# Kernel tuning notes

Measured on AMD Instinct MI355X. Metric: run time of the kernel, lower is better.

The kernel has to match this reference:

```python
import jax, jax.numpy as jnp
import numpy as np

B, S, D, H = 8, 1024, 1024, 16
HD = D // H  # head dim 64

def setup_inputs() -> dict:
    key = jax.random.key(0)
    ks = jax.random.split(key, 7)
    def w(k):
        return jax.random.normal(k, (D, D), dtype=jnp.float32) * (1.0 / np.sqrt(D))
    return {
        'q': jax.random.normal(ks[0], (B, S, D), dtype=jnp.float32),
        'k': jax.random.normal(ks[1], (B, S, D), dtype=jnp.float32),
        'v': jax.random.normal(ks[2], (B, S, D), dtype=jnp.float32),
        'Wq': w(ks[3]), 'Wk': w(ks[4]), 'Wv': w(ks[5]), 'Wo': w(ks[6]),
    }

def reference(q, k, v, Wq, Wk, Wv, Wo):
    # projections (nn.Linear, no bias): y = x @ W.T
    def heads(x, W):
        return (x @ W.T).reshape(B, S, H, HD)
    qh, kh, vh = heads(q, Wq), heads(k, Wk), heads(v, Wv)
    scale = 1.0 / np.sqrt(HD).astype(np.float32)
    scores = jnp.einsum('bqhd,bkhd->bhqk', qh, kh) * scale  # [B,H,S,S]
    # masked=True -> causal mask
    causal = jnp.tril(jnp.ones((S, S), dtype=bool))
    scores = jnp.where(causal[None, None], scores, jnp.float32(-1e9))
    attn = jax.nn.softmax(scores, axis=-1)
    out = jnp.einsum('bhqk,bkhd->bqhd', attn, vh).reshape(B, S, D)
    return out @ Wo.T
```

## Files before the change

kernel.cpp:

```cpp
#include <hip/hip_runtime.h>
#include <hip/hip_bf16.h>

#define B_ 8
#define S_ 1024
#define D_ 1024
#define H_ 16
#define HD_ 64
#define M_ (B_*S_)
#define NQB (S_/128)

typedef __attribute__((ext_vector_type(8))) short short8;
typedef __attribute__((ext_vector_type(4))) short short4v;
typedef __attribute__((ext_vector_type(4))) float f32x4;
typedef __attribute__((ext_vector_type(16))) float f32x16;
typedef __attribute__((ext_vector_type(4))) int int4v;
typedef __attribute__((ext_vector_type(2))) int int2v;

#define CSC 0.18033688f

__device__ __forceinline__ unsigned short f2bf(float f) {
    unsigned int u = __float_as_uint(f);
    u += 0x7FFF + ((u >> 16) & 1);
    return (unsigned short)(u >> 16);
}

__device__ __forceinline__ void gload16(const void* g, void* l) {
    __builtin_amdgcn_global_load_lds(
        (const __attribute__((address_space(1))) void*)g,
        (__attribute__((address_space(3))) void*)l, 16, 0, 0);
}

__device__ __forceinline__ int2v plswap(int a, int b) {
    return __builtin_amdgcn_permlane32_swap(a, b, false, false);
}

__device__ __forceinline__ float max3f(float a, float b, float c) {
    return fmaxf(fmaxf(a, b), c);
}

struct CvtArgs { const float* src[28]; unsigned short* dst[28]; };

__global__ __launch_bounds__(256)
void cvt_w(CvtArgs a)
{
    const int y = blockIdx.y;
    const float* __restrict__ src = a.src[y];
    unsigned short* __restrict__ dst = a.dst[y];
    int i = blockIdx.x * 256 + threadIdx.x;
    float4 x = reinterpret_cast<const float4*>(src)[i*2];
    float4 z = reinterpret_cast<const float4*>(src)[i*2+1];
    short8 v = short8{(short)f2bf(x.x),(short)f2bf(x.y),(short)f2bf(x.z),(short)f2bf(x.w),
                      (short)f2bf(z.x),(short)f2bf(z.y),(short)f2bf(z.z),(short)f2bf(z.w)};
    reinterpret_cast<short8*>(dst)[i] = v;
}

__device__ __forceinline__ void gemm_core_bf16A(
    const unsigned short* __restrict__ A, const unsigned short* __restrict__ Wb,
    short* lds, int m0, int n0, int tid, f32x4 (&acc)[4][4])
{
    const int K = D_;
    const int lane = tid & 63, wave = tid >> 6;
    const int wr = wave >> 1, wc = wave & 1;
    const int r16 = lane & 15, g4 = lane >> 4;
    const int srow = lane >> 3;
    const int scol = ((lane ^ srow) & 7) * 8;

    #define STAGE(t, bi)                                                      \
        { _Pragma("unroll")                                                   \
          for (int c = 0; c < 4; ++c) {                                       \
              int chunk = wave*4 + c;                                         \
              gload16(Wb + (size_t)(n0 + chunk*8 + srow) * K + (t)*64 + scol, \
                      lds + (bi)*16384 + 8192 + chunk*512);                   \
              gload16(A + (size_t)(m0 + chunk*8 + srow) * K + (t)*64 + scol,  \
                      lds + (bi)*16384 + chunk*512);                          \
          } }

    STAGE(0, 0);

    const int NT = K / 64;
    for (int t = 0; t < NT; ++t) {
        const int cur = t & 1;
        if (t + 1 < NT) {
            STAGE(t+1, cur^1);
            asm volatile("s_waitcnt vmcnt(8)" ::: "memory");
        } else {
            asm volatile("s_waitcnt vmcnt(0)" ::: "memory");
        }
        __builtin_amdgcn_s_barrier();

        const short* Ab = lds + cur*16384;
        const short* Bb = Ab + 8192;
        #pragma unroll
        for (int ks = 0; ks < 2; ++ks) {
            short8 af[4], bf[4];
            #pragma unroll
            for (int m = 0; m < 4; ++m) {
                int r = wr*64 + m*16 + r16;
                af[m] = *reinterpret_cast<const short8*>(
                    &Ab[r*64 + (((ks*4 + g4) ^ (r16 & 7)) << 3)]);
            }
            #pragma unroll
            for (int n = 0; n < 4; ++n) {
                int r = wc*64 + n*16 + r16;
                bf[n] = *reinterpret_cast<const short8*>(
                    &Bb[r*64 + (((ks*4 + g4) ^ (r16 & 7)) << 3)]);
            }
            __builtin_amdgcn_s_setprio(1);
            #pragma unroll
            for (int m = 0; m < 4; ++m)
                #pragma unroll
                for (int n = 0; n < 4; ++n)
                    acc[m][n] = __builtin_amdgcn_mfma_f32_16x16x32_bf16(af[m], bf[n], acc[m][n], 0, 0, 0);
            __builtin_amdgcn_s_setprio(0);
        }
        __builtin_amdgcn_s_barrier();
    }
    #undef STAGE
}

template<int MODE>
__device__ __forceinline__ void epilogue_vec(
    float* Cl, void* __restrict__ Ov, int m0, int n0, int tid, f32x4 (&acc)[4][4])
{
    const int N = D_;
    const int lane = tid & 63, wave = tid >> 6;
    const int wr = wave >> 1, wc = wave & 1;
    const int r16 = lane & 15, g4 = lane >> 4;

    #pragma unroll
    for (int p = 0; p < 2; ++p) {
        if (p) __syncthreads();
        if (wr == p) {
            #pragma unroll
            for (int m = 0; m < 4; ++m)
                #pragma unroll
                for (int n = 0; n < 4; ++n)
                    #pragma unroll
                    for (int i = 0; i < 4; ++i)
                        Cl[(m*16 + g4*4 + i)*132 + wc*64 + n*16 + r16] = acc[m][n][i];
        }
        __syncthreads();
        if (MODE == 1) {
            #pragma unroll
            for (int j = 0; j < 8; ++j) {
                int c = j*256 + tid;
                int row = c >> 5, cg = c & 31;
                float4 val = *reinterpret_cast<const float4*>(&Cl[row*132 + cg*4]);
                *reinterpret_cast<float4*>(
                    &((float*)Ov)[(size_t)(m0 + p*64 + row)*N + n0 + cg*4]) = val;
            }
        } else {
            #pragma unroll
            for (int j = 0; j < 4; ++j) {
                int c2 = j*256 + tid;
                int row = c2 >> 4, col = (c2 & 15)*8;
                float4 a = *reinterpret_cast<const float4*>(&Cl[row*132 + col]);
                float4 bq = *reinterpret_cast<const float4*>(&Cl[row*132 + col + 4]);
                if (MODE == 3) {
                    a.x *= CSC; a.y *= CSC; a.z *= CSC; a.w *= CSC;
                    bq.x *= CSC; bq.y *= CSC; bq.z *= CSC; bq.w *= CSC;
                }
                short8 v = short8{(short)f2bf(a.x),(short)f2bf(a.y),(short)f2bf(a.z),(short)f2bf(a.w),
                                  (short)f2bf(bq.x),(short)f2bf(bq.y),(short)f2bf(bq.z),(short)f2bf(bq.w)};
                *reinterpret_cast<short8*>(
                    &((unsigned short*)Ov)[(size_t)(m0 + p*64 + row)*N + n0 + col]) = v;
            }
        }
    }
}

struct ProjArgs {
    const unsigned short* A[3];
    const unsigned short* W[3];
    void* O[3];
};

__global__ __launch_bounds__(256)
void gemm_proj(ProjArgs pa)
{
    __shared__ __align__(16) short lds[32768];

    const int L = blockIdx.x;
    const int which = L >> 9;
    const int inner = L & 511;
    const int xcd = inner & 7, jj = inner >> 3;
    const int m0 = ((xcd << 3) | (jj & 7)) * 128;
    const int n0 = (jj >> 3) * 128;
    const int tid = threadIdx.x;

    f32x4 acc[4][4] = {};
    gemm_core_bf16A(pa.A[which], pa.W[which], lds, m0, n0, tid, acc);

    if (which == 2) {
        const int lane = tid & 63, wave = tid >> 6;
        const int wr = wave >> 1, wc = wave & 1;
        const int r16 = lane & 15, g4 = lane >> 4;
        #pragma unroll
        for (int m = 0; m < 4; ++m) {
            int row0 = m0 + wr*64 + m*16 + g4*4;
            #pragma unroll
            for (int n = 0; n < 4; ++n) {
                int col = n0 + wc*64 + n*16 + r16;
                size_t vrow = (size_t)((row0 >> 10)*16 + (col >> 6))*64 + (col & 63);
                short4v pk = short4v{(short)f2bf(acc[m][n][0]), (short)f2bf(acc[m][n][1]),
                                     (short)f2bf(acc[m][n][2]), (short)f2bf(acc[m][n][3])};
                *reinterpret_cast<short4v*>((unsigned short*)pa.O[2] + vrow*S_ + (row0 & 1023)) = pk;
            }
        }
    } else if (which == 0) {
        epilogue_vec<3>((float*)lds, pa.O[0], m0, n0, tid, acc);
    } else {
        epilogue_vec<0>((float*)lds, pa.O[1], m0, n0, tid, acc);
    }
}

__global__ __launch_bounds__(256)
void gemm_final(const unsigned short* __restrict__ A, const unsigned short* __restrict__ Wb,
                float* __restrict__ Ov)
{
    __shared__ __align__(16) short lds[32768];

    const int L = blockIdx.x;
    const int xcd = L & 7, jj = L >> 3;
    const int m0 = ((xcd << 3) | (jj & 7)) * 128;
    const int n0 = (jj >> 3) * 128;
    const int tid = threadIdx.x;

    f32x4 acc[4][4] = {};
    gemm_core_bf16A(A, Wb, lds, m0, n0, tid, acc);
    epilogue_vec<1>((float*)lds, Ov, m0, n0, tid, acc);
}

__global__ __launch_bounds__(256)
void attn_fwd(const unsigned short* __restrict__ Qh,
              const unsigned short* __restrict__ Kh,
              const unsigned short* __restrict__ VtG,
              unsigned short* __restrict__ AO)
{
    __shared__ __align__(16) short Kl[2][64*64];
    __shared__ __align__(16) short Vl[2][64*64];

    const int tid  = threadIdx.x;
    const int lane = tid & 63, wave = tid >> 6;
    const int l31 = lane & 31, h32 = lane >> 5;
    const int L = blockIdx.x;
    const int xcd = L & 7, jj = L >> 3;
    const int pr = jj & 3;
    const int hb = xcd*16 + (jj >> 2);
    const int h = hb & 15, b = hb >> 4;

    const int slot = tid & 7;
    const int r0 = tid >> 3, r1 = r0 + 32;
    const int koff0 = r0*64 + ((slot ^ (r0 & 7)) << 3);
    const int koff1 = r1*64 + ((slot ^ (r1 & 7)) << 3);

    const unsigned short* Kg0 = Kh + ((size_t)b*S_)*D_ + h*HD_;
    const unsigned short* Vg0 = VtG + ((size_t)(b*H_ + h)*HD_)*S_;

    for (int t = 0; t < 2; ++t) {
        const int qb = t ? pr : (NQB - 1 - pr);
        const int q0w = qb*128 + wave*32;
        const int qi  = q0w + l31;

        short8 qf[4];
        #pragma unroll
        for (int m = 0; m < 4; ++m)
            qf[m] = *reinterpret_cast<const short8*>(
                Qh + ((size_t)b*S_ + qi)*D_ + h*HD_ + m*16 + h32*8);

        f32x16 o0 = {}, o1 = {};
        float mrow = -1e30f, lsum = 0.f;
        const int nkb = 2*qb + 2;

        short8 ka, kc, va, vc;
        ka = *reinterpret_cast<const short8*>(Kg0 + (size_t)r0*D_ + slot*8);
        kc = *reinterpret_cast<const short8*>(Kg0 + (size_t)r1*D_ + slot*8);
        va = *reinterpret_cast<const short8*>(Vg0 + (size_t)r0*S_ + slot*8);
        vc = *reinterpret_cast<const short8*>(Vg0 + (size_t)r1*S_ + slot*8);
        *reinterpret_cast<short8*>(&Kl[0][koff0]) = ka;
        *reinterpret_cast<short8*>(&Kl[0][koff1]) = kc;
        *reinterpret_cast<short8*>(&Vl[0][koff0]) = va;
        *reinterpret_cast<short8*>(&Vl[0][koff1]) = vc;
        __syncthreads();

        for (int kb = 0; kb < nkb; ++kb) {
            const int cur = kb & 1;
            const bool havenext = (kb + 1 < nkb);
            if (havenext) {
                const unsigned short* Kg = Kg0 + (size_t)(kb+1)*64*D_;
                const unsigned short* Vg = Vg0 + (kb+1)*64;
                ka = *reinterpret_cast<const short8*>(Kg + (size_t)r0*D_ + slot*8);
                kc = *reinterpret_cast<const short8*>(Kg + (size_t)r1*D_ + slot*8);
                va = *reinterpret_cast<const short8*>(Vg + (size_t)r0*S_ + slot*8);
                vc = *reinterpret_cast<const short8*>(Vg + (size_t)r1*S_ + slot*8);
            }

            if (kb*64 <= q0w + 31) {
                f32x16 p0 = {}, p1 = {};
                __builtin_amdgcn_s_setprio(1);
                #pragma unroll
                for (int m = 0; m < 4; ++m) {
                    short8 kf0 = *reinterpret_cast<const short8*>(
                        &Kl[cur][l31*64 + ((((m<<1)|h32) ^ (l31 & 7)) << 3)]);
                    short8 kf1 = *reinterpret_cast<const short8*>(
                        &Kl[cur][(32 + l31)*64 + ((((m<<1)|h32) ^ (l31 & 7)) << 3)]);
                    p0 = __builtin_amdgcn_mfma_f32_32x32x16_bf16(kf0, qf[m], p0, 0, 0, 0);
                    p1 = __builtin_amdgcn_mfma_f32_32x32x16_bf16(kf1, qf[m], p1, 0, 0, 0);
                }
                __builtin_amdgcn_s_setprio(0);

                if (kb*64 + 63 > q0w) {
                    #pragma unroll
                    for (int r = 0; r < 16; ++r) {
                        int kk = (r & 3) + ((r >> 2) << 3) + (h32 << 2);
                        if (kb*64      + kk > qi) p0[r] = -1e30f;
                        if (kb*64 + 32 + kk > qi) p1[r] = -1e30f;
                    }
                }

                float t0 = max3f(p0[0],  p0[1],  p0[2]);
                float t1 = max3f(p0[3],  p0[4],  p0[5]);
                float t2 = max3f(p0[6],  p0[7],  p0[8]);
                float t3 = max3f(p0[9],  p0[10], p0[11]);
                float t4 = max3f(p0[12], p0[13], p0[14]);
                float t5 = max3f(p0[15], p1[0],  p1[1]);
                float t6 = max3f(p1[2],  p1[3],  p1[4]);
                float t7 = max3f(p1[5],  p1[6],  p1[7]);
                float t8 = max3f(p1[8],  p1[9],  p1[10]);
                float t9 = max3f(p1[11], p1[12], p1[13]);
                float ta = fmaxf(p1[14], p1[15]);
                float mloc = fmaxf(max3f(max3f(t0,t1,t2), max3f(t3,t4,t5), max3f(t6,t7,t8)),
                                   fmaxf(t9, ta));
                int2v mm = plswap(__float_as_int(mloc), __float_as_int(mloc));
                float pm = fmaxf(__int_as_float(mm.x), __int_as_float(mm.y));

                if (__any(pm > mrow + 11.5416f)) {
                    float mn = fmaxf(mrow, pm);
                    float so = exp2f(mrow - mn);
                    #pragma unroll
                    for (int r = 0; r < 16; ++r) { o0[r] *= so; o1[r] *= so; }
                    lsum *= so;
                    mrow = mn;
                }

                #pragma unroll
                for (int r = 0; r < 16; ++r) p0[r] = exp2f(p0[r] - mrow);
                #pragma unroll
                for (int r = 0; r < 16; ++r) p1[r] = exp2f(p1[r] - mrow);
                float sq[8];
                #pragma unroll
                for (int r = 0; r < 8; ++r)
                    sq[r] = (p0[2*r] + p0[2*r+1]) + (p1[2*r] + p1[2*r+1]);
                float rs = ((sq[0]+sq[1]) + (sq[2]+sq[3])) + ((sq[4]+sq[5]) + (sq[6]+sq[7]));
                int2v ss = plswap(__float_as_int(rs), __float_as_int(rs));
                lsum += __int_as_float(ss.x) + __int_as_float(ss.y);

                #pragma unroll
                for (int m = 0; m < 4; ++m) {
                    const int mb = (m & 1) * 8;
                    unsigned int C0, C1, C2, C3;
                    if (m < 2) {
                        asm("v_cvt_pk_bf16_f32 %0, %1, %2" : "=v"(C0) : "v"(p0[mb+0]), "v"(p0[mb+1]));
                        asm("v_cvt_pk_bf16_f32 %0, %1, %2" : "=v"(C1) : "v"(p0[mb+2]), "v"(p0[mb+3]));
                        asm("v_cvt_pk_bf16_f32 %0, %1, %2" : "=v"(C2) : "v"(p0[mb+4]), "v"(p0[mb+5]));
                        asm("v_cvt_pk_bf16_f32 %0, %1, %2" : "=v"(C3) : "v"(p0[mb+6]), "v"(p0[mb+7]));
                    } else {
                        asm("v_cvt_pk_bf16_f32 %0, %1, %2" : "=v"(C0) : "v"(p1[mb+0]), "v"(p1[mb+1]));
                        asm("v_cvt_pk_bf16_f32 %0, %1, %2" : "=v"(C1) : "v"(p1[mb+2]), "v"(p1[mb+3]));
                        asm("v_cvt_pk_bf16_f32 %0, %1, %2" : "=v"(C2) : "v"(p1[mb+4]), "v"(p1[mb+5]));
                        asm("v_cvt_pk_bf16_f32 %0, %1, %2" : "=v"(C3) : "v"(p1[mb+6]), "v"(p1[mb+7]));
                    }
                    int2v s0 = plswap((int)C0, (int)C2);
                    int2v s1 = plswap((int)C1, (int)C3);
                    int4v wi; wi.x = s0.x; wi.y = s1.x; wi.z = s0.y; wi.w = s1.y;
                    short8 pf = __builtin_bit_cast(short8, wi);

                    short8 vf0 = *reinterpret_cast<const short8*>(
                        &Vl[cur][l31*64 + ((((m<<1)|h32) ^ (l31 & 7)) << 3)]);
                    short8 vf1 = *reinterpret_cast<const short8*>(
                        &Vl[cur][(32 + l31)*64 + ((((m<<1)|h32) ^ (l31 & 7)) << 3)]);
                    o0 = __builtin_amdgcn_mfma_f32_32x32x16_bf16(vf0, pf, o0, 0, 0, 0);
                    o1 = __builtin_amdgcn_mfma_f32_32x32x16_bf16(vf1, pf, o1, 0, 0, 0);
                }
            }

            if (havenext) {
                const int nb = cur ^ 1;
                *reinterpret_cast<short8*>(&Kl[nb][koff0]) = ka;
                *reinterpret_cast<short8*>(&Kl[nb][koff1]) = kc;
                *reinterpret_cast<short8*>(&Vl[nb][koff0]) = va;
                *reinterpret_cast<short8*>(&Vl[nb][koff1]) = vc;
            }
            __syncthreads();
        }

        float inv = 1.f / lsum;
        #pragma unroll
        for (int tt = 0; tt < 2; ++tt) {
            #pragma unroll
            for (int g = 0; g < 4; ++g) {
                short4v pk;
                #pragma unroll
                for (int j = 0; j < 4; ++j) {
                    float val = (tt ? o1[g*4+j] : o0[g*4+j]) * inv;
                    pk[j] = (short)f2bf(val);
                }
                int d = tt*32 + g*8 + h32*4;
                *reinterpret_cast<short4v*>(AO + ((size_t)b*S_ + qi)*D_ + h*HD_ + d) = pk;
            }
        }
    }
}

extern "C" void kernel_launch(void* const* d_in, const int* in_sizes, int n_in,
                              void* d_out, int out_size, void* d_ws, size_t ws_size,
                              hipStream_t stream) {
    const float* q  = (const float*)d_in[0];
    const float* k  = (const float*)d_in[1];
    const float* v  = (const float*)d_in[2];
    const float* Wq = (const float*)d_in[3];
    const float* Wk = (const float*)d_in[4];
    const float* Wv = (const float*)d_in[5];
    const float* Wo = (const float*)d_in[6];

    unsigned short* Wqb = (unsigned short*)d_ws;
    unsigned short* Wkb = Wqb + (size_t)D_*D_;
    unsigned short* Wvb = Wkb + (size_t)D_*D_;
    unsigned short* Wob = Wvb + (size_t)D_*D_;
    unsigned short* Qh  = Wob + (size_t)D_*D_;
    unsigned short* Kh  = Qh  + (size_t)M_*D_;
    unsigned short* VtG = Kh  + (size_t)M_*D_;
    unsigned short* Qb  = VtG + (size_t)M_*D_;
    unsigned short* Kb  = Qb  + (size_t)M_*D_;
    unsigned short* Vb  = Kb  + (size_t)M_*D_;
    unsigned short* AO  = Qb;

    dim3 blk(256);

    CvtArgs ca;
    ca.src[0] = Wq; ca.dst[0] = Wqb;
    ca.src[1] = Wk; ca.dst[1] = Wkb;
    ca.src[2] = Wv; ca.dst[2] = Wvb;
    ca.src[3] = Wo; ca.dst[3] = Wob;
    const float* qkv_src[3] = {q, k, v};
    unsigned short* qkv_dst[3] = {Qb, Kb, Vb};
    for (int mtx = 0; mtx < 3; ++mtx)
        for (int c = 0; c < 8; ++c) {
            ca.src[4 + mtx*8 + c] = qkv_src[mtx] + (size_t)c*1048576;
            ca.dst[4 + mtx*8 + c] = qkv_dst[mtx] + (size_t)c*1048576;
        }
    cvt_w<<<dim3(512, 28), blk, 0, stream>>>(ca);

    ProjArgs pa;
    pa.A[0] = Qb; pa.W[0] = Wqb; pa.O[0] = Qh;
    pa.A[1] = Kb; pa.W[1] = Wkb; pa.O[1] = Kh;
    pa.A[2] = Vb; pa.W[2] = Wvb; pa.O[2] = VtG;
    gemm_proj<<<dim3(1536), blk, 0, stream>>>(pa);

    attn_fwd<<<dim3(512), blk, 0, stream>>>(Qh, Kh, VtG, AO);

    gemm_final<<<dim3(512), blk, 0, stream>>>(AO, Wob, (float*)d_out);
}
```

Baseline: 162.3 us.

## Process paired causal query blocks jointly sharing K/V tiles with async LDS loads

The attention kernel used to run its high and low query blocks one after the other, streaming K/V twice. It now runs both in a single pass over the key blocks, so each K/V tile loaded into LDS feeds both query blocks. Global-to-LDS copies now go through gload16 (async direct-to-LDS), with the swizzle moved to the source address. Launch bounds now request 2 blocks per SM, and the conversion kernel handles 4 floats per thread over twice as many blocks. The cost is higher register pressure from two sets of accumulators and softmax state, which may cause spills under the occupancy hint.

```diff
diff --git a/kernel.cpp b/kernel.cpp
--- a/kernel.cpp
+++ b/kernel.cpp
@@ -47,11 +47,9 @@
     const float* __restrict__ src = a.src[y];
     unsigned short* __restrict__ dst = a.dst[y];
     int i = blockIdx.x * 256 + threadIdx.x;
-    float4 x = reinterpret_cast<const float4*>(src)[i*2];
-    float4 z = reinterpret_cast<const float4*>(src)[i*2+1];
-    short8 v = short8{(short)f2bf(x.x),(short)f2bf(x.y),(short)f2bf(x.z),(short)f2bf(x.w),
-                      (short)f2bf(z.x),(short)f2bf(z.y),(short)f2bf(z.z),(short)f2bf(z.w)};
-    reinterpret_cast<short8*>(dst)[i] = v;
+    float4 x = reinterpret_cast<const float4*>(src)[i];
+    short4v v = short4v{(short)f2bf(x.x),(short)f2bf(x.y),(short)f2bf(x.z),(short)f2bf(x.w)};
+    reinterpret_cast<short4v*>(dst)[i] = v;
 }
 
 __device__ __forceinline__ void gemm_core_bf16A(
@@ -231,7 +229,7 @@
     epilogue_vec<1>((float*)lds, Ov, m0, n0, tid, acc);
 }
 
-__global__ __launch_bounds__(256)
+__global__ __launch_bounds__(256, 2)
 void attn_fwd(const unsigned short* __restrict__ Qh,
               const unsigned short* __restrict__ Kh,
               const unsigned short* __restrict__ VtG,
@@ -251,165 +249,187 @@
 
     const int slot = tid & 7;
     const int r0 = tid >> 3, r1 = r0 + 32;
-    const int koff0 = r0*64 + ((slot ^ (r0 & 7)) << 3);
-    const int koff1 = r1*64 + ((slot ^ (r1 & 7)) << 3);
+    const int sc8 = ((slot ^ (r0 & 7)) << 3);
 
     const unsigned short* Kg0 = Kh + ((size_t)b*S_)*D_ + h*HD_;
     const unsigned short* Vg0 = VtG + ((size_t)(b*H_ + h)*HD_)*S_;
 
-    for (int t = 0; t < 2; ++t) {
-        const int qb = t ? pr : (NQB - 1 - pr);
-        const int q0w = qb*128 + wave*32;
-        const int qi  = q0w + l31;
-
-        short8 qf[4];
-        #pragma unroll
-        for (int m = 0; m < 4; ++m)
-            qf[m] = *reinterpret_cast<const short8*>(
-                Qh + ((size_t)b*S_ + qi)*D_ + h*HD_ + m*16 + h32*8);
-
-        f32x16 o0 = {}, o1 = {};
-        float mrow = -1e30f, lsum = 0.f;
-        const int nkb = 2*qb + 2;
-
-        short8 ka, kc, va, vc;
-        ka = *reinterpret_cast<const short8*>(Kg0 + (size_t)r0*D_ + slot*8);
-        kc = *reinterpret_cast<const short8*>(Kg0 + (size_t)r1*D_ + slot*8);
-        va = *reinterpret_cast<const short8*>(Vg0 + (size_t)r0*S_ + slot*8);
-        vc = *reinterpret_cast<const short8*>(Vg0 + (size_t)r1*S_ + slot*8);
-        *reinterpret_cast<short8*>(&Kl[0][koff0]) = ka;
-        *reinterpret_cast<short8*>(&Kl[0][koff1]) = kc;
-        *reinterpret_cast<short8*>(&Vl[0][koff0]) = va;
-        *reinterpret_cast<short8*>(&Vl[0][koff1]) = vc;
+    #define STAGEKV(kb1, nb)                                                  \
+        { const unsigned short* Kg = Kg0 + (size_t)(kb1)*64*D_;               \
+          const unsigned short* Vg = Vg0 + (size_t)(kb1)*64;                  \
+          gload16(Kg + (size_t)r0*D_ + sc8, &Kl[nb][r0*64 + slot*8]);         \
+          gload16(Kg + (size_t)r1*D_ + sc8, &Kl[nb][r1*64 + slot*8]);         \
+          gload16(Vg + (size_t)r0*S_ + sc8, &Vl[nb][r0*64 + slot*8]);         \
+          gload16(Vg + (size_t)r1*S_ + sc8, &Vl[nb][r1*64 + slot*8]); }
+
+    const int qbH = NQB - 1 - pr;
+    const int qbL = pr;
+    const int q0wH = qbH*128 + wave*32, qiH = q0wH + l31;
+    const int q0wL = qbL*128 + wave*32, qiL = q0wL + l31;
+
+    short8 qfH[4], qfL[4];
+    #pragma unroll
+    for (int m = 0; m < 4; ++m) {
+        qfH[m] = *reinterpret_cast<const short8*>(
+            Qh + ((size_t)b*S_ + qiH)*D_ + h*HD_ + m*16 + h32*8);
+        qfL[m] = *reinterpret_cast<const short8*>(
+            Qh + ((size_t)b*S_ + qiL)*D_ + h*HD_ + m*16 + h32*8);
+    }
+
+    f32x16 oH0 = {}, oH1 = {}, oL0 = {}, oL1 = {};
+    float mH = -1e30f, lH = 0.f, mL = -1e30f, lL = 0.f;
+    const int nkb = 2*qbH + 2;
+
+    STAGEKV(0, 0);
+    asm volatile("s_waitcnt vmcnt(0)" ::: "memory");
+    __syncthreads();
+
+    #define MASK_G(p0, p1, q0w, qi)                                           \
+        if (kb*64 + 63 > (q0w)) {                                             \
+            _Pragma("unroll")                                                 \
+            for (int r = 0; r < 16; ++r) {                                    \
+                int kk = (r & 3) + ((r >> 2) << 3) + (h32 << 2);              \
+                if (kb*64      + kk > (qi)) p0[r] = -1e30f;                   \
+                if (kb*64 + 32 + kk > (qi)) p1[r] = -1e30f;                   \
+            } }
+
+    #define SOFTMAX_G(p0, p1, mrow, lsum, o0, o1) {                           \
+        float t0 = max3f(p0[0],  p0[1],  p0[2]);                              \
+        float t1 = max3f(p0[3],  p0[4],  p0[5]);                              \
+        float t2 = max3f(p0[6],  p0[7],  p0[8]);                              \
+        float t3 = max3f(p0[9],  p0[10], p0[11]);                             \
+        float t4 = max3f(p0[12], p0[13], p0[14]);                             \
+        float t5 = max3f(p0[15], p1[0],  p1[1]);                              \
+        float t6 = max3f(p1[2],  p1[3],  p1[4]);                              \
+        float t7 = max3f(p1[5],  p1[6],  p1[7]);                              \
+        float t8 = max3f(p1[8],  p1[9],  p1[10]);                             \
+        float t9 = max3f(p1[11], p1[12], p1[13]);                             \
+        float ta = fmaxf(p1[14], p1[15]);                                     \
+        float mloc = fmaxf(max3f(max3f(t0,t1,t2), max3f(t3,t4,t5),            \
+                                 max3f(t6,t7,t8)), fmaxf(t9, ta));            \
+        int2v mm = plswap(__float_as_int(mloc), __float_as_int(mloc));        \
+        float pm = fmaxf(__int_as_float(mm.x), __int_as_float(mm.y));         \
+        if (__any(pm > mrow + 11.5416f)) {                                    \
+            float mn = fmaxf(mrow, pm);                                       \
+            float so = exp2f(mrow - mn);                                      \
+            _Pragma("unroll")                                                 \
+            for (int r = 0; r < 16; ++r) { o0[r] *= so; o1[r] *= so; }        \
+            lsum *= so;                                                       \
+            mrow = mn;                                                        \
+        }                                                                     \
+        _Pragma("unroll")                                                     \
+        for (int r = 0; r < 16; ++r) p0[r] = exp2f(p0[r] - mrow);             \
+        _Pragma("unroll")                                                     \
+        for (int r = 0; r < 16; ++r) p1[r] = exp2f(p1[r] - mrow);             \
+        float sq[8];                                                          \
+        _Pragma("unroll")                                                     \
+        for (int r = 0; r < 8; ++r)                                           \
+            sq[r] = (p0[2*r] + p0[2*r+1]) + (p1[2*r] + p1[2*r+1]);            \
+        float rs = ((sq[0]+sq[1]) + (sq[2]+sq[3])) + ((sq[4]+sq[5]) + (sq[6]+sq[7])); \
+        int2v ss = plswap(__float_as_int(rs), __float_as_int(rs));            \
+        lsum += __int_as_float(ss.x) + __int_as_float(ss.y); }
+
+    #define PF_G(p0, p1, m, pf) {                                             \
+        const int mb = ((m) & 1) * 8;                                         \
+        unsigned int C0, C1, C2, C3;                                          \
+        if ((m) < 2) {                                                        \
+            asm("v_cvt_pk_bf16_f32 %0, %1, %2" : "=v"(C0) : "v"(p0[mb+0]), "v"(p0[mb+1])); \
+            asm("v_cvt_pk_bf16_f32 %0, %1, %2" : "=v"(C1) : "v"(p0[mb+2]), "v"(p0[mb+3])); \
+            asm("v_cvt_pk_bf16_f32 %0, %1, %2" : "=v"(C2) : "v"(p0[mb+4]), "v"(p0[mb+5])); \
+            asm("v_cvt_pk_bf16_f32 %0, %1, %2" : "=v"(C3) : "v"(p0[mb+6]), "v"(p0[mb+7])); \
+        } else {                                                              \
+            asm("v_cvt_pk_bf16_f32 %0, %1, %2" : "=v"(C0) : "v"(p1[mb+0]), "v"(p1[mb+1])); \
+            asm("v_cvt_pk_bf16_f32 %0, %1, %2" : "=v"(C1) : "v"(p1[mb+2]), "v"(p1[mb+3])); \
+            asm("v_cvt_pk_bf16_f32 %0, %1, %2" : "=v"(C2) : "v"(p1[mb+4]), "v"(p1[mb+5])); \
+            asm("v_cvt_pk_bf16_f32 %0, %1, %2" : "=v"(C3) : "v"(p1[mb+6]), "v"(p1[mb+7])); \
+        }                                                                     \
+        int2v s0 = plswap((int)C0, (int)C2);                                  \
+        int2v s1 = plswap((int)C1, (int)C3);                                  \
+        int4v wi; wi.x = s0.x; wi.y = s1.x; wi.z = s0.y; wi.w = s1.y;         \
+        pf = __builtin_bit_cast(short8, wi); }
+
+    for (int kb = 0; kb < nkb; ++kb) {
+        const int cur = kb & 1;
+        const bool havenext = (kb + 1 < nkb);
+        if (havenext) STAGEKV(kb+1, cur^1);
+
+        const bool actH = (kb*64 <= q0wH + 31);
+        const bool actL = (kb*64 <= q0wL + 31);
+
+        if (actH) {
+            f32x16 pH0 = {}, pH1 = {}, pL0 = {}, pL1 = {};
+            __builtin_amdgcn_s_setprio(1);
+            #pragma unroll
+            for (int m = 0; m < 4; ++m) {
+                short8 kf0 = *reinterpret_cast<const short8*>(
+                    &Kl[cur][l31*64 + ((((m<<1)|h32) ^ (l31 & 7)) << 3)]);
+                short8 kf1 = *reinterpret_cast<const short8*>(
+                    &Kl[cur][(32 + l31)*64 + ((((m<<1)|h32) ^ (l31 & 7)) << 3)]);
+                pH0 = __builtin_amdgcn_mfma_f32_32x32x16_bf16(kf0, qfH[m], pH0, 0, 0, 0);
+                pH1 = __builtin_amdgcn_mfma_f32_32x32x16_bf16(kf1, qfH[m], pH1, 0, 0, 0);
+                if (actL) {
+                    pL0 = __builtin_amdgcn_mfma_f32_32x32x16_bf16(kf0, qfL[m], pL0, 0, 0, 0);
+                    pL1 = __builtin_amdgcn_mfma_f32_32x32x16_bf16(kf1, qfL[m], pL1, 0, 0, 0);
+                }
+            }
+            __builtin_amdgcn_s_setprio(0);
+
+            MASK_G(pH0, pH1, q0wH, qiH);
+            SOFTMAX_G(pH0, pH1, mH, lH, oH0, oH1);
+            if (actL) {
+                MASK_G(pL0, pL1, q0wL, qiL);
+                SOFTMAX_G(pL0, pL1, mL, lL, oL0, oL1);
+            }
+
+            __builtin_amdgcn_s_setprio(1);
+            #pragma unroll
+            for (int m = 0; m < 4; ++m) {
+                short8 vf0 = *reinterpret_cast<const short8*>(
+                    &Vl[cur][l31*64 + ((((m<<1)|h32) ^ (l31 & 7)) << 3)]);
+                short8 vf1 = *reinterpret_cast<const short8*>(
+                    &Vl[cur][(32 + l31)*64 + ((((m<<1)|h32) ^ (l31 & 7)) << 3)]);
+                {
+                    short8 pf; PF_G(pH0, pH1, m, pf);
+                    oH0 = __builtin_amdgcn_mfma_f32_32x32x16_bf16(vf0, pf, oH0, 0, 0, 0);
+                    oH1 = __builtin_amdgcn_mfma_f32_32x32x16_bf16(vf1, pf, oH1, 0, 0, 0);
+                }
+                if (actL) {
+                    short8 pf; PF_G(pL0, pL1, m, pf);
+                    oL0 = __builtin_amdgcn_mfma_f32_32x32x16_bf16(vf0, pf, oL0, 0, 0, 0);
+                    oL1 = __builtin_amdgcn_mfma_f32_32x32x16_bf16(vf1, pf, oL1, 0, 0, 0);
+                }
+            }
+            __builtin_amdgcn_s_setprio(0);
+        }
+
+        asm volatile("s_waitcnt vmcnt(0)" ::: "memory");
         __syncthreads();
-
-        for (int kb = 0; kb < nkb; ++kb) {
-            const int cur = kb & 1;
-            const bool havenext = (kb + 1 < nkb);
-            if (havenext) {
-                const unsigned short* Kg = Kg0 + (size_t)(kb+1)*64*D_;
-                const unsigned short* Vg = Vg0 + (kb+1)*64;
-                ka = *reinterpret_cast<const short8*>(Kg + (size_t)r0*D_ + slot*8);
-                kc = *reinterpret_cast<const short8*>(Kg + (size_t)r1*D_ + slot*8);
-                va = *reinterpret_cast<const short8*>(Vg + (size_t)r0*S_ + slot*8);
-                vc = *reinterpret_cast<const short8*>(Vg + (size_t)r1*S_ + slot*8);
-            }
-
-            if (kb*64 <= q0w + 31) {
-                f32x16 p0 = {}, p1 = {};
-                __builtin_amdgcn_s_setprio(1);
-                #pragma unroll
-                for (int m = 0; m < 4; ++m) {
-                    short8 kf0 = *reinterpret_cast<const short8*>(
-                        &Kl[cur][l31*64 + ((((m<<1)|h32) ^ (l31 & 7)) << 3)]);
-                    short8 kf1 = *reinterpret_cast<const short8*>(
-                        &Kl[cur][(32 + l31)*64 + ((((m<<1)|h32) ^ (l31 & 7)) << 3)]);
-                    p0 = __builtin_amdgcn_mfma_f32_32x32x16_bf16(kf0, qf[m], p0, 0, 0, 0);
-                    p1 = __builtin_amdgcn_mfma_f32_32x32x16_bf16(kf1, qf[m], p1, 0, 0, 0);
-                }
-                __builtin_amdgcn_s_setprio(0);
-
-                if (kb*64 + 63 > q0w) {
-                    #pragma unroll
-                    for (int r = 0; r < 16; ++r) {
-                        int kk = (r & 3) + ((r >> 2) << 3) + (h32 << 2);
-                        if (kb*64      + kk > qi) p0[r] = -1e30f;
-                        if (kb*64 + 32 + kk > qi) p1[r] = -1e30f;
-                    }
-                }
-
-                float t0 = max3f(p0[0],  p0[1],  p0[2]);
-                float t1 = max3f(p0[3],  p0[4],  p0[5]);
-                float t2 = max3f(p0[6],  p0[7],  p0[8]);
-                float t3 = max3f(p0[9],  p0[10], p0[11]);
-                float t4 = max3f(p0[12], p0[13], p0[14]);
-                float t5 = max3f(p0[15], p1[0],  p1[1]);
-                float t6 = max3f(p1[2],  p1[3],  p1[4]);
-                float t7 = max3f(p1[5],  p1[6],  p1[7]);
-                float t8 = max3f(p1[8],  p1[9],  p1[10]);
-                float t9 = max3f(p1[11], p1[12], p1[13]);
-                float ta = fmaxf(p1[14], p1[15]);
-                float mloc = fmaxf(max3f(max3f(t0,t1,t2), max3f(t3,t4,t5), max3f(t6,t7,t8)),
-                                   fmaxf(t9, ta));
-                int2v mm = plswap(__float_as_int(mloc), __float_as_int(mloc));
-                float pm = fmaxf(__int_as_float(mm.x), __int_as_float(mm.y));
-
-                if (__any(pm > mrow + 11.5416f)) {
-                    float mn = fmaxf(mrow, pm);
-                    float so = exp2f(mrow - mn);
-                    #pragma unroll
-                    for (int r = 0; r < 16; ++r) { o0[r] *= so; o1[r] *= so; }
-                    lsum *= so;
-                    mrow = mn;
-                }
-
-                #pragma unroll
-                for (int r = 0; r < 16; ++r) p0[r] = exp2f(p0[r] - mrow);
-                #pragma unroll
-                for (int r = 0; r < 16; ++r) p1[r] = exp2f(p1[r] - mrow);
-                float sq[8];
-                #pragma unroll
-                for (int r = 0; r < 8; ++r)
-                    sq[r] = (p0[2*r] + p0[2*r+1]) + (p1[2*r] + p1[2*r+1]);
-                float rs = ((sq[0]+sq[1]) + (sq[2]+sq[3])) + ((sq[4]+sq[5]) + (sq[6]+sq[7]));
-                int2v ss = plswap(__float_as_int(rs), __float_as_int(rs));
-                lsum += __int_as_float(ss.x) + __int_as_float(ss.y);
-
-                #pragma unroll
-                for (int m = 0; m < 4; ++m) {
-                    const int mb = (m & 1) * 8;
-                    unsigned int C0, C1, C2, C3;
-                    if (m < 2) {
-                        asm("v_cvt_pk_bf16_f32 %0, %1, %2" : "=v"(C0) : "v"(p0[mb+0]), "v"(p0[mb+1]));
-                        asm("v_cvt_pk_bf16_f32 %0, %1, %2" : "=v"(C1) : "v"(p0[mb+2]), "v"(p0[mb+3]));
-                        asm("v_cvt_pk_bf16_f32 %0, %1, %2" : "=v"(C2) : "v"(p0[mb+4]), "v"(p0[mb+5]));
-                        asm("v_cvt_pk_bf16_f32 %0, %1, %2" : "=v"(C3) : "v"(p0[mb+6]), "v"(p0[mb+7]));
-                    } else {
-                        asm("v_cvt_pk_bf16_f32 %0, %1, %2" : "=v"(C0) : "v"(p1[mb+0]), "v"(p1[mb+1]));
-                        asm("v_cvt_pk_bf16_f32 %0, %1, %2" : "=v"(C1) : "v"(p1[mb+2]), "v"(p1[mb+3]));
-                        asm("v_cvt_pk_bf16_f32 %0, %1, %2" : "=v"(C2) : "v"(p1[mb+4]), "v"(p1[mb+5]));
-                        asm("v_cvt_pk_bf16_f32 %0, %1, %2" : "=v"(C3) : "v"(p1[mb+6]), "v"(p1[mb+7]));
-                    }
-                    int2v s0 = plswap((int)C0, (int)C2);
-                    int2v s1 = plswap((int)C1, (int)C3);
-                    int4v wi; wi.x = s0.x; wi.y = s1.x; wi.z = s0.y; wi.w = s1.y;
-                    short8 pf = __builtin_bit_cast(short8, wi);
-
-                    short8 vf0 = *reinterpret_cast<const short8*>(
-                        &Vl[cur][l31*64 + ((((m<<1)|h32) ^ (l31 & 7)) << 3)]);
-                    short8 vf1 = *reinterpret_cast<const short8*>(
-                        &Vl[cur][(32 + l31)*64 + ((((m<<1)|h32) ^ (l31 & 7)) << 3)]);
-                    o0 = __builtin_amdgcn_mfma_f32_32x32x16_bf16(vf0, pf, o0, 0, 0, 0);
-                    o1 = __builtin_amdgcn_mfma_f32_32x32x16_bf16(vf1, pf, o1, 0, 0, 0);
-                }
-            }
-
-            if (havenext) {
-                const int nb = cur ^ 1;
-                *reinterpret_cast<short8*>(&Kl[nb][koff0]) = ka;
-                *reinterpret_cast<short8*>(&Kl[nb][koff1]) = kc;
-                *reinterpret_cast<short8*>(&Vl[nb][koff0]) = va;
-                *reinterpret_cast<short8*>(&Vl[nb][koff1]) = vc;
-            }
-            __syncthreads();
-        }
-
-        float inv = 1.f / lsum;
-        #pragma unroll
-        for (int tt = 0; tt < 2; ++tt) {
-            #pragma unroll
-            for (int g = 0; g < 4; ++g) {
-                short4v pk;
-                #pragma unroll
-                for (int j = 0; j < 4; ++j) {
-                    float val = (tt ? o1[g*4+j] : o0[g*4+j]) * inv;
-                    pk[j] = (short)f2bf(val);
-                }
-                int d = tt*32 + g*8 + h32*4;
-                *reinterpret_cast<short4v*>(AO + ((size_t)b*S_ + qi)*D_ + h*HD_ + d) = pk;
-            }
-        }
     }
+
+    #define WRITEO(o0, o1, lsum, qi) {                                        \
+        float inv = 1.f / (lsum);                                             \
+        _Pragma("unroll")                                                     \
+        for (int tt = 0; tt < 2; ++tt) {                                      \
+            _Pragma("unroll")                                                 \
+            for (int g = 0; g < 4; ++g) {                                     \
+                short4v pk;                                                   \
+                _Pragma("unroll")                                             \
+                for (int j = 0; j < 4; ++j) {                                 \
+                    float val = (tt ? o1[g*4+j] : o0[g*4+j]) * inv;           \
+                    pk[j] = (short)f2bf(val);                                 \
+                }                                                             \
+                int d = tt*32 + g*8 + h32*4;                                  \
+                *reinterpret_cast<short4v*>(AO + ((size_t)b*S_ + (qi))*D_ + h*HD_ + d) = pk; \
+            } } }
+
+    WRITEO(oH0, oH1, lH, qiH);
+    WRITEO(oL0, oL1, lL, qiL);
+
+    #undef STAGEKV
+    #undef MASK_G
+    #undef SOFTMAX_G
+    #undef PF_G
+    #undef WRITEO
 }
 
 extern "C" void kernel_launch(void* const* d_in, const int* in_sizes, int n_in,
@@ -449,7 +469,7 @@
             ca.src[4 + mtx*8 + c] = qkv_src[mtx] + (size_t)c*1048576;
             ca.dst[4 + mtx*8 + c] = qkv_dst[mtx] + (size_t)c*1048576;
         }
-    cvt_w<<<dim3(512, 28), blk, 0, stream>>>(ca);
+    cvt_w<<<dim3(1024, 28), blk, 0, stream>>>(ca);
 
     ProjArgs pa;
     pa.A[0] = Qb; pa.W[0] = Wqb; pa.O[0] = Qh;
```

After: 160.5 us. About the same (-1.1%).

## Split attention work into one query block per workgroup with async LDS loads

Applied to the files above, without the earlier changes.

The attention kernel now launches one workgroup per (batch, head, query-block) rather than pairing a long and a short query block per workgroup, which doubles the grid. K/V tiles are staged with direct global-to-LDS loads (gload16) using a swizzled source address instead of a register round-trip, and launch bounds request higher occupancy. The conversion kernel is also changed to process 4 floats per thread with twice the grid. The finer split aims to improve load balance and latency hiding, at the cost of per-block Q loads and loss of the explicit causal pairing balance.

```diff
diff --git a/kernel.cpp b/kernel.cpp
--- a/kernel.cpp
+++ b/kernel.cpp
@@ -47,11 +47,9 @@
     const float* __restrict__ src = a.src[y];
     unsigned short* __restrict__ dst = a.dst[y];
     int i = blockIdx.x * 256 + threadIdx.x;
-    float4 x = reinterpret_cast<const float4*>(src)[i*2];
-    float4 z = reinterpret_cast<const float4*>(src)[i*2+1];
-    short8 v = short8{(short)f2bf(x.x),(short)f2bf(x.y),(short)f2bf(x.z),(short)f2bf(x.w),
-                      (short)f2bf(z.x),(short)f2bf(z.y),(short)f2bf(z.z),(short)f2bf(z.w)};
-    reinterpret_cast<short8*>(dst)[i] = v;
+    float4 x = reinterpret_cast<const float4*>(src)[i];
+    short4v v = short4v{(short)f2bf(x.x),(short)f2bf(x.y),(short)f2bf(x.z),(short)f2bf(x.w)};
+    reinterpret_cast<short4v*>(dst)[i] = v;
 }
 
 __device__ __forceinline__ void gemm_core_bf16A(
@@ -231,7 +229,7 @@
     epilogue_vec<1>((float*)lds, Ov, m0, n0, tid, acc);
 }
 
-__global__ __launch_bounds__(256)
+__global__ __launch_bounds__(256, 4)
 void attn_fwd(const unsigned short* __restrict__ Qh,
               const unsigned short* __restrict__ Kh,
               const unsigned short* __restrict__ VtG,
@@ -244,172 +242,158 @@
     const int lane = tid & 63, wave = tid >> 6;
     const int l31 = lane & 31, h32 = lane >> 5;
     const int L = blockIdx.x;
-    const int xcd = L & 7, jj = L >> 3;
-    const int pr = jj & 3;
-    const int hb = xcd*16 + (jj >> 2);
+    const int xcd = L & 7, inner = L >> 3;
+    const int hb = xcd*16 + (inner >> 3);
     const int h = hb & 15, b = hb >> 4;
+    const int qsel = inner & 7;
+    const int qb = (qsel & 1) ? (qsel >> 1) : (7 - (qsel >> 1));
 
     const int slot = tid & 7;
     const int r0 = tid >> 3, r1 = r0 + 32;
-    const int koff0 = r0*64 + ((slot ^ (r0 & 7)) << 3);
-    const int koff1 = r1*64 + ((slot ^ (r1 & 7)) << 3);
+    const int sc8 = ((slot ^ (r0 & 7)) << 3);
 
     const unsigned short* Kg0 = Kh + ((size_t)b*S_)*D_ + h*HD_;
     const unsigned short* Vg0 = VtG + ((size_t)(b*H_ + h)*HD_)*S_;
 
-    for (int t = 0; t < 2; ++t) {
-        const int qb = t ? pr : (NQB - 1 - pr);
-        const int q0w = qb*128 + wave*32;
-        const int qi  = q0w + l31;
-
-        short8 qf[4];
+    #define STAGEKV(kb1, nb)                                                  \
+        { const unsigned short* Kg = Kg0 + (size_t)(kb1)*64*D_;               \
+          const unsigned short* Vg = Vg0 + (size_t)(kb1)*64;                  \
+          gload16(Kg + (size_t)r0*D_ + sc8, &Kl[nb][r0*64 + slot*8]);         \
+          gload16(Kg + (size_t)r1*D_ + sc8, &Kl[nb][r1*64 + slot*8]);         \
+          gload16(Vg + (size_t)r0*S_ + sc8, &Vl[nb][r0*64 + slot*8]);         \
+          gload16(Vg + (size_t)r1*S_ + sc8, &Vl[nb][r1*64 + slot*8]); }
+
+    const int q0w = qb*128 + wave*32;
+    const int qi  = q0w + l31;
+
+    short8 qf[4];
+    #pragma unroll
+    for (int m = 0; m < 4; ++m)
+        qf[m] = *reinterpret_cast<const short8*>(
+            Qh + ((size_t)b*S_ + qi)*D_ + h*HD_ + m*16 + h32*8);
+
+    f32x16 o0 = {}, o1 = {};
+    float mrow = -1e30f, lsum = 0.f;
+    const int nkb = 2*qb + 2;
+
+    STAGEKV(0, 0);
+    asm volatile("s_waitcnt vmcnt(0)" ::: "memory");
+    __syncthreads();
+
+    for (int kb = 0; kb < nkb; ++kb) {
+        const int cur = kb & 1;
+        const bool havenext = (kb + 1 < nkb);
+        if (havenext) STAGEKV(kb+1, cur^1);
+
+        if (kb*64 <= q0w + 31) {
+            f32x16 p0 = {}, p1 = {};
+            __builtin_amdgcn_s_setprio(1);
+            #pragma unroll
+            for (int m = 0; m < 4; ++m) {
+                short8 kf0 = *reinterpret_cast<const short8*>(
+                    &Kl[cur][l31*64 + ((((m<<1)|h32) ^ (l31 & 7)) << 3)]);
+                short8 kf1 = *reinterpret_cast<const short8*>(
+                    &Kl[cur][(32 + l31)*64 + ((((m<<1)|h32) ^ (l31 & 7)) << 3)]);
+                p0 = __builtin_amdgcn_mfma_f32_32x32x16_bf16(kf0, qf[m], p0, 0, 0, 0);
+                p1 = __builtin_amdgcn_mfma_f32_32x32x16_bf16(kf1, qf[m], p1, 0, 0, 0);
+            }
+            __builtin_amdgcn_s_setprio(0);
+
+            if (kb*64 + 63 > q0w) {
+                #pragma unroll
+                for (int r = 0; r < 16; ++r) {
+                    int kk = (r & 3) + ((r >> 2) << 3) + (h32 << 2);
+                    if (kb*64      + kk > qi) p0[r] = -1e30f;
+                    if (kb*64 + 32 + kk > qi) p1[r] = -1e30f;
+                }
+            }
+
+            float t0 = max3f(p0[0],  p0[1],  p0[2]);
+            float t1 = max3f(p0[3],  p0[4],  p0[5]);
+            float t2 = max3f(p0[6],  p0[7],  p0[8]);
+            float t3 = max3f(p0[9],  p0[10], p0[11]);
+            float t4 = max3f(p0[12], p0[13], p0[14]);
+            float t5 = max3f(p0[15], p1[0],  p1[1]);
+            float t6 = max3f(p1[2],  p1[3],  p1[4]);
+            float t7 = max3f(p1[5],  p1[6],  p1[7]);
+            float t8 = max3f(p1[8],  p1[9],  p1[10]);
+            float t9 = max3f(p1[11], p1[12], p1[13]);
+            float ta = fmaxf(p1[14], p1[15]);
+            float mloc = fmaxf(max3f(max3f(t0,t1,t2), max3f(t3,t4,t5), max3f(t6,t7,t8)),
+                               fmaxf(t9, ta));
+            int2v mm = plswap(__float_as_int(mloc), __float_as_int(mloc));
+            float pm = fmaxf(__int_as_float(mm.x), __int_as_float(mm.y));
+
+            if (__any(pm > mrow + 11.5416f)) {
+                float mn = fmaxf(mrow, pm);
+                float so = exp2f(mrow - mn);
+                #pragma unroll
+                for (int r = 0; r < 16; ++r) { o0[r] *= so; o1[r] *= so; }
+                lsum *= so;
+                mrow = mn;
+            }
+
+            #pragma unroll
+            for (int r = 0; r < 16; ++r) p0[r] = exp2f(p0[r] - mrow);
+            #pragma unroll
+            for (int r = 0; r < 16; ++r) p1[r] = exp2f(p1[r] - mrow);
+            float sq[8];
+            #pragma unroll
+            for (int r = 0; r < 8; ++r)
+                sq[r] = (p0[2*r] + p0[2*r+1]) + (p1[2*r] + p1[2*r+1]);
+            float rs = ((sq[0]+sq[1]) + (sq[2]+sq[3])) + ((sq[4]+sq[5]) + (sq[6]+sq[7]));
+            int2v ss = plswap(__float_as_int(rs), __float_as_int(rs));
+            lsum += __int_as_float(ss.x) + __int_as_float(ss.y);
+
+            #pragma unroll
+            for (int m = 0; m < 4; ++m) {
+                const int mb = (m & 1) * 8;
+                unsigned int C0, C1, C2, C3;
+                if (m < 2) {
+                    asm("v_cvt_pk_bf16_f32 %0, %1, %2" : "=v"(C0) : "v"(p0[mb+0]), "v"(p0[mb+1]));
+                    asm("v_cvt_pk_bf16_f32 %0, %1, %2" : "=v"(C1) : "v"(p0[mb+2]), "v"(p0[mb+3]));
+                    asm("v_cvt_pk_bf16_f32 %0, %1, %2" : "=v"(C2) : "v"(p0[mb+4]), "v"(p0[mb+5]));
+                    asm("v_cvt_pk_bf16_f32 %0, %1, %2" : "=v"(C3) : "v"(p0[mb+6]), "v"(p0[mb+7]));
+                } else {
+                    asm("v_cvt_pk_bf16_f32 %0, %1, %2" : "=v"(C0) : "v"(p1[mb+0]), "v"(p1[mb+1]));
+                    asm("v_cvt_pk_bf16_f32 %0, %1, %2" : "=v"(C1) : "v"(p1[mb+2]), "v"(p1[mb+3]));
+                    asm("v_cvt_pk_bf16_f32 %0, %1, %2" : "=v"(C2) : "v"(p1[mb+4]), "v"(p1[mb+5]));
+                    asm("v_cvt_pk_bf16_f32 %0, %1, %2" : "=v"(C3) : "v"(p1[mb+6]), "v"(p1[mb+7]));
+                }
+                int2v s0 = plswap((int)C0, (int)C2);
+                int2v s1 = plswap((int)C1, (int)C3);
+                int4v wi; wi.x = s0.x; wi.y = s1.x; wi.z = s0.y; wi.w = s1.y;
+                short8 pf = __builtin_bit_cast(short8, wi);
+
+                short8 vf0 = *reinterpret_cast<const short8*>(
+                    &Vl[cur][l31*64 + ((((m<<1)|h32) ^ (l31 & 7)) << 3)]);
+                short8 vf1 = *reinterpret_cast<const short8*>(
+                    &Vl[cur][(32 + l31)*64 + ((((m<<1)|h32) ^ (l31 & 7)) << 3)]);
+                o0 = __builtin_amdgcn_mfma_f32_32x32x16_bf16(vf0, pf, o0, 0, 0, 0);
+                o1 = __builtin_amdgcn_mfma_f32_32x32x16_bf16(vf1, pf, o1, 0, 0, 0);
+            }
+        }
+
+        asm volatile("s_waitcnt vmcnt(0)" ::: "memory");
+        __syncthreads();
+    }
+
+    float inv = 1.f / lsum;
+    #pragma unroll
+    for (int tt = 0; tt < 2; ++tt) {
         #pragma unroll
-        for (int m = 0; m < 4; ++m)
-            qf[m] = *reinterpret_cast<const short8*>(
-                Qh + ((size_t)b*S_ + qi)*D_ + h*HD_ + m*16 + h32*8);
-
-        f32x16 o0 = {}, o1 = {};
-        float mrow = -1e30f, lsum = 0.f;
-        const int nkb = 2*qb + 2;
-
-        short8 ka, kc, va, vc;
-        ka = *reinterpret_cast<const short8*>(Kg0 + (size_t)r0*D_ + slot*8);
-        kc = *reinterpret_cast<const short8*>(Kg0 + (size_t)r1*D_ + slot*8);
-        va = *reinterpret_cast<const short8*>(Vg0 + (size_t)r0*S_ + slot*8);
-        vc = *reinterpret_cast<const short8*>(Vg0 + (size_t)r1*S_ + slot*8);
-        *reinterpret_cast<short8*>(&Kl[0][koff0]) = ka;
-        *reinterpret_cast<short8*>(&Kl[0][koff1]) = kc;
-        *reinterpret_cast<short8*>(&Vl[0][koff0]) = va;
-        *reinterpret_cast<short8*>(&Vl[0][koff1]) = vc;
-        __syncthreads();
-
-        for (int kb = 0; kb < nkb; ++kb) {
-            const int cur = kb & 1;
-            const bool havenext = (kb + 1 < nkb);
-            if (havenext) {
-                const unsigned short* Kg = Kg0 + (size_t)(kb+1)*64*D_;
-                const unsigned short* Vg = Vg0 + (kb+1)*64;
-                ka = *reinterpret_cast<const short8*>(Kg + (size_t)r0*D_ + slot*8);
-                kc = *reinterpret_cast<const short8*>(Kg + (size_t)r1*D_ + slot*8);
-                va = *reinterpret_cast<const short8*>(Vg + (size_t)r0*S_ + slot*8);
-                vc = *reinterpret_cast<const short8*>(Vg + (size_t)r1*S_ + slot*8);
-            }
-
-            if (kb*64 <= q0w + 31) {
-                f32x16 p0 = {}, p1 = {};
-                __builtin_amdgcn_s_setprio(1);
-                #pragma unroll
-                for (int m = 0; m < 4; ++m) {
-                    short8 kf0 = *reinterpret_cast<const short8*>(
-                        &Kl[cur][l31*64 + ((((m<<1)|h32) ^ (l31 & 7)) << 3)]);
-                    short8 kf1 = *reinterpret_cast<const short8*>(
-                        &Kl[cur][(32 + l31)*64 + ((((m<<1)|h32) ^ (l31 & 7)) << 3)]);
-                    p0 = __builtin_amdgcn_mfma_f32_32x32x16_bf16(kf0, qf[m], p0, 0, 0, 0);
-                    p1 = __builtin_amdgcn_mfma_f32_32x32x16_bf16(kf1, qf[m], p1, 0, 0, 0);
-                }
-                __builtin_amdgcn_s_setprio(0);
-
-                if (kb*64 + 63 > q0w) {
-                    #pragma unroll
-                    for (int r = 0; r < 16; ++r) {
-                        int kk = (r & 3) + ((r >> 2) << 3) + (h32 << 2);
-                        if (kb*64      + kk > qi) p0[r] = -1e30f;
-                        if (kb*64 + 32 + kk > qi) p1[r] = -1e30f;
-                    }
-                }
-
-                float t0 = max3f(p0[0],  p0[1],  p0[2]);
-                float t1 = max3f(p0[3],  p0[4],  p0[5]);
-                float t2 = max3f(p0[6],  p0[7],  p0[8]);
-                float t3 = max3f(p0[9],  p0[10], p0[11]);
-                float t4 = max3f(p0[12], p0[13], p0[14]);
-                float t5 = max3f(p0[15], p1[0],  p1[1]);
-                float t6 = max3f(p1[2],  p1[3],  p1[4]);
-                float t7 = max3f(p1[5],  p1[6],  p1[7]);
-                float t8 = max3f(p1[8],  p1[9],  p1[10]);
-                float t9 = max3f(p1[11], p1[12], p1[13]);
-                float ta = fmaxf(p1[14], p1[15]);
-                float mloc = fmaxf(max3f(max3f(t0,t1,t2), max3f(t3,t4,t5), max3f(t6,t7,t8)),
-                                   fmaxf(t9, ta));
-                int2v mm = plswap(__float_as_int(mloc), __float_as_int(mloc));
-                float pm = fmaxf(__int_as_float(mm.x), __int_as_float(mm.y));
-
-                if (__any(pm > mrow + 11.5416f)) {
-                    float mn = fmaxf(mrow, pm);
-                    float so = exp2f(mrow - mn);
-                    #pragma unroll
-                    for (int r = 0; r < 16; ++r) { o0[r] *= so; o1[r] *= so; }
-                    lsum *= so;
-                    mrow = mn;
-                }
-
-                #pragma unroll
-                for (int r = 0; r < 16; ++r) p0[r] = exp2f(p0[r] - mrow);
-                #pragma unroll
-                for (int r = 0; r < 16; ++r) p1[r] = exp2f(p1[r] - mrow);
-                float sq[8];
-                #pragma unroll
-                for (int r = 0; r < 8; ++r)
-                    sq[r] = (p0[2*r] + p0[2*r+1]) + (p1[2*r] + p1[2*r+1]);
-                float rs = ((sq[0]+sq[1]) + (sq[2]+sq[3])) + ((sq[4]+sq[5]) + (sq[6]+sq[7]));
-                int2v ss = plswap(__float_as_int(rs), __float_as_int(rs));
-                lsum += __int_as_float(ss.x) + __int_as_float(ss.y);
-
-                #pragma unroll
-                for (int m = 0; m < 4; ++m) {
-                    const int mb = (m & 1) * 8;
-                    unsigned int C0, C1, C2, C3;
-                    if (m < 2) {
-                        asm("v_cvt_pk_bf16_f32 %0, %1, %2" : "=v"(C0) : "v"(p0[mb+0]), "v"(p0[mb+1]));
-                        asm("v_cvt_pk_bf16_f32 %0, %1, %2" : "=v"(C1) : "v"(p0[mb+2]), "v"(p0[mb+3]));
-                        asm("v_cvt_pk_bf16_f32 %0, %1, %2" : "=v"(C2) : "v"(p0[mb+4]), "v"(p0[mb+5]));
-                        asm("v_cvt_pk_bf16_f32 %0, %1, %2" : "=v"(C3) : "v"(p0[mb+6]), "v"(p0[mb+7]));
-                    } else {
-                        asm("v_cvt_pk_bf16_f32 %0, %1, %2" : "=v"(C0) : "v"(p1[mb+0]), "v"(p1[mb+1]));
-                        asm("v_cvt_pk_bf16_f32 %0, %1, %2" : "=v"(C1) : "v"(p1[mb+2]), "v"(p1[mb+3]));
-                        asm("v_cvt_pk_bf16_f32 %0, %1, %2" : "=v"(C2) : "v"(p1[mb+4]), "v"(p1[mb+5]));
-                        asm("v_cvt_pk_bf16_f32 %0, %1, %2" : "=v"(C3) : "v"(p1[mb+6]), "v"(p1[mb+7]));
-                    }
-                    int2v s0 = plswap((int)C0, (int)C2);
-                    int2v s1 = plswap((int)C1, (int)C3);
-                    int4v wi; wi.x = s0.x; wi.y = s1.x; wi.z = s0.y; wi.w = s1.y;
-                    short8 pf = __builtin_bit_cast(short8, wi);
-
-                    short8 vf0 = *reinterpret_cast<const short8*>(
-                        &Vl[cur][l31*64 + ((((m<<1)|h32) ^ (l31 & 7)) << 3)]);
-                    short8 vf1 = *reinterpret_cast<const short8*>(
-                        &Vl[cur][(32 + l31)*64 + ((((m<<1)|h32) ^ (l31 & 7)) << 3)]);
-                    o0 = __builtin_amdgcn_mfma_f32_32x32x16_bf16(vf0, pf, o0, 0, 0, 0);
-                    o1 = __builtin_amdgcn_mfma_f32_32x32x16_bf16(vf1, pf, o1, 0, 0, 0);
-                }
-            }
-
-            if (havenext) {
-                const int nb = cur ^ 1;
-                *reinterpret_cast<short8*>(&Kl[nb][koff0]) = ka;
-                *reinterpret_cast<short8*>(&Kl[nb][koff1]) = kc;
-                *reinterpret_cast<short8*>(&Vl[nb][koff0]) = va;
-                *reinterpret_cast<short8*>(&Vl[nb][koff1]) = vc;
-            }
-            __syncthreads();
-        }
-
-        float inv = 1.f / lsum;
-        #pragma unroll
-        for (int tt = 0; tt < 2; ++tt) {
-            #pragma unroll
-            for (int g = 0; g < 4; ++g) {
-                short4v pk;
-                #pragma unroll
-                for (int j = 0; j < 4; ++j) {
-                    float val = (tt ? o1[g*4+j] : o0[g*4+j]) * inv;
-                    pk[j] = (short)f2bf(val);
-                }
-                int d = tt*32 + g*8 + h32*4;
-                *reinterpret_cast<short4v*>(AO + ((size_t)b*S_ + qi)*D_ + h*HD_ + d) = pk;
-            }
+        for (int g = 0; g < 4; ++g) {
+            short4v pk;
+            #pragma unroll
+            for (int j = 0; j < 4; ++j) {
+                float val = (tt ? o1[g*4+j] : o0[g*4+j]) * inv;
+                pk[j] = (short)f2bf(val);
+            }
+            int d = tt*32 + g*8 + h32*4;
+            *reinterpret_cast<short4v*>(AO + ((size_t)b*S_ + qi)*D_ + h*HD_ + d) = pk;
         }
     }
+    #undef STAGEKV
 }
 
 extern "C" void kernel_launch(void* const* d_in, const int* in_sizes, int n_in,
@@ -449,7 +433,7 @@
             ca.src[4 + mtx*8 + c] = qkv_src[mtx] + (size_t)c*1048576;
             ca.dst[4 + mtx*8 + c] = qkv_dst[mtx] + (size_t)c*1048576;
         }
-    cvt_w<<<dim3(512, 28), blk, 0, stream>>>(ca);
+    cvt_w<<<dim3(1024, 28), blk, 0, stream>>>(ca);
 
     ProjArgs pa;
     pa.A[0] = Qb; pa.W[0] = Wqb; pa.O[0] = Qh;
@@ -457,7 +441,7 @@
     pa.A[2] = Vb; pa.W[2] = Wvb; pa.O[2] = VtG;
     gemm_proj<<<dim3(1536), blk, 0, stream>>>(pa);
 
-    attn_fwd<<<dim3(512), blk, 0, stream>>>(Qh, Kh, VtG, AO);
+    attn_fwd<<<dim3(1024), blk, 0, stream>>>(Qh, Kh, VtG, AO);
 
     gemm_final<<<dim3(512), blk, 0, stream>>>(AO, Wob, (float*)d_out);
 }
```

New measurement: 170.7 us. 5.2% more time.
